# Kernel tuning notes

Hardware: AMD Instinct MI355X
Metric: run time of the kernel (lower is better)

The kernel has to match this reference:

```python
import jax, jax.numpy as jnp
import numpy as np

B = 131072   # batch
K = 3        # kernel size (= stride)
NP = 9       # num patches (9x9 image, 3x3 kernel, stride 3)
NU = 81      # num logic units/kernels
NOPS = 16    # real-valued binary logic ops


def setup_inputs() -> dict:
    key = jax.random.key(0)
    k1, k2, k3, k4 = jax.random.split(key, 4)
    x = jax.random.uniform(k1, (B, 1, 9, 9), dtype=jnp.float32)          # soft-binary image
    sel_a_logits = jax.random.normal(k2, (NU, K * K), dtype=jnp.float32)  # input-A selector per unit
    sel_b_logits = jax.random.normal(k3, (NU, K * K), dtype=jnp.float32)  # input-B selector per unit
    op_logits = jax.random.normal(k4, (NU, NOPS), dtype=jnp.float32)      # logic-op mixture per unit
    return {"x": x, "sel_a_logits": sel_a_logits, "sel_b_logits": sel_b_logits, "op_logits": op_logits}


def _soft_logic_mix(a, b, w):
    # a, b: [B, NU] soft-binary operands; w: [NU, 16] op mixture weights (broadcast over batch).
    # The 16 real-valued binary logic gates (Petersen et al. differentiable logic networks).
    ab = a * b
    return (w[:, 1] * ab
            + w[:, 2] * (a - ab)
            + w[:, 3] * a
            + w[:, 4] * (b - ab)
            + w[:, 5] * b
            + w[:, 6] * (a + b - 2.0 * ab)      # xor
            + w[:, 7] * (a + b - ab)            # or
            + w[:, 8] * (1.0 - (a + b - ab))    # nor
            + w[:, 9] * (1.0 - (a + b - 2.0 * ab))  # xnor
            + w[:, 10] * (1.0 - b)
            + w[:, 11] * (1.0 - b + ab)
            + w[:, 12] * (1.0 - a)
            + w[:, 13] * (1.0 - a + ab)
            + w[:, 14] * (1.0 - ab)             # nand
            + w[:, 15])                          # op 0 contributes 0


def reference(x, sel_a_logits, sel_b_logits, op_logits):
    b_sz = x.shape[0]
    img = x[:, 0]  # [B, 9, 9]
    # unfold(2,K,S).unfold(3,K,S) with S == K == 3 -> non-overlapping 3x3 patches, row-major patch order
    patches = img.reshape(b_sz, NP // K, K, NP // K, K)
    patches = patches.transpose(0, 1, 3, 2, 4).reshape(b_sz, NP, K * K)  # [B, 9, 9]
    # unit u uses patch u // kernels_per_pos (kernels_per_pos = 81 // 9 = 9)
    unit2patch = jnp.arange(NU) // (NU // NP)
    inp = patches[:, unit2patch]  # [B, 81, 9]
    a = jnp.einsum('bui,ui->bu', inp, jax.nn.softmax(sel_a_logits, axis=-1))  # [B, 81]
    b = jnp.einsum('bui,ui->bu', inp, jax.nn.softmax(sel_b_logits, axis=-1))  # [B, 81]
    w = jax.nn.softmax(op_logits, axis=-1)  # [81, 16]
    return _soft_logic_mix(a, b, w)  # [B, 81]
```

## Files before the change

### kernel.cpp

```cpp
#include <hip/hip_runtime.h>
#include <math.h>


#define NB      131072
#define NUNITS  81
#define BPB     64
#define THREADS 256
#define NBLK    (NB / BPB)
#define REC     24
#define CHUNKS  1296

__global__ __launch_bounds__(THREADS)
void logic_conv2d_kernel(const float* __restrict__ x,
                         const float* __restrict__ sa_logits,
                         const float* __restrict__ sb_logits,
                         const float* __restrict__ op_logits,
                         float* __restrict__ out)
{
    __shared__ float s_in [BPB * 81];
    __shared__ float s_out[BPB * 81];
    __shared__ float s_tab[NUNITS * REC];

    const int tid  = threadIdx.x;
    const int lane = tid & 63;
    const int wave = tid >> 6;
    const size_t b0 = (size_t)blockIdx.x * BPB;

    {
        const float4* gsrc = (const float4*)(x + b0 * 81);
        float4* s4 = (float4*)s_in;
        #pragma unroll
        for (int k = 0; k < 6; ++k) {
            int j = tid + k * THREADS;
            if (j < CHUNKS) s4[j] = gsrc[j];
        }
    }

    if (tid < 81) {
        const int u = tid;
        float v[9], m = -1e30f;
        #pragma unroll
        for (int i = 0; i < 9; ++i) { v[i] = sa_logits[u * 9 + i]; m = fmaxf(m, v[i]); }
        float s = 0.f;
        #pragma unroll
        for (int i = 0; i < 9; ++i) { v[i] = expf(v[i] - m); s += v[i]; }
        const float r = 1.f / s;
        #pragma unroll
        for (int i = 0; i < 9; ++i) s_tab[u * REC + i] = v[i] * r;
    } else if (tid < 162) {
        const int u = tid - 81;
        float v[9], m = -1e30f;
        #pragma unroll
        for (int i = 0; i < 9; ++i) { v[i] = sb_logits[u * 9 + i]; m = fmaxf(m, v[i]); }
        float s = 0.f;
        #pragma unroll
        for (int i = 0; i < 9; ++i) { v[i] = expf(v[i] - m); s += v[i]; }
        const float r = 1.f / s;
        #pragma unroll
        for (int i = 0; i < 9; ++i) s_tab[u * REC + 9 + i] = v[i] * r;
    } else if (tid < 243) {
        const int u = tid - 162;
        float v[16], m = -1e30f;
        #pragma unroll
        for (int i = 0; i < 16; ++i) { v[i] = op_logits[u * 16 + i]; m = fmaxf(m, v[i]); }
        float s = 0.f;
        #pragma unroll
        for (int i = 0; i < 16; ++i) { v[i] = expf(v[i] - m); s += v[i]; }
        const float r = 1.f / s;
        #pragma unroll
        for (int i = 0; i < 16; ++i) v[i] *= r;
        const float cab = v[1] - v[2] - v[4] - 2.f*v[6] - v[7] + v[8] + 2.f*v[9]
                        + v[11] + v[13] - v[14];
        const float ca  = v[2] + v[3] + v[6] + v[7] - v[8] - v[9] - v[12] - v[13];
        const float cb  = v[4] + v[5] + v[6] + v[7] - v[8] - v[9] - v[10] - v[11];
        const float c0  = v[8] + v[9] + v[10] + v[11] + v[12] + v[13] + v[14] + v[15];
        s_tab[u * REC + 18] = cab;
        s_tab[u * REC + 19] = ca;
        s_tab[u * REC + 20] = cb;
        s_tab[u * REC + 21] = c0;
    }

    __syncthreads();

    {
        const float* my_in = s_in + lane * 81;
        for (int u = wave; u < NUNITS; u += 4) {
            const int p    = u / 9;
            const int base = (p / 3) * 27 + (p % 3) * 3;
            const float i0 = my_in[base + 0],  i1 = my_in[base + 1],  i2 = my_in[base + 2];
            const float i3 = my_in[base + 9],  i4 = my_in[base + 10], i5 = my_in[base + 11];
            const float i6 = my_in[base + 18], i7 = my_in[base + 19], i8 = my_in[base + 20];
            const float* wr = s_tab + u * REC;
            const float a = i0*wr[0] + i1*wr[1] + i2*wr[2]
                          + i3*wr[3] + i4*wr[4] + i5*wr[5]
                          + i6*wr[6] + i7*wr[7] + i8*wr[8];
            const float b = i0*wr[9]  + i1*wr[10] + i2*wr[11]
                          + i3*wr[12] + i4*wr[13] + i5*wr[14]
                          + i6*wr[15] + i7*wr[16] + i8*wr[17];
            const float res = wr[21] + wr[19]*a + wr[20]*b + wr[18]*(a*b);
            s_out[lane * 81 + u] = res;
        }
    }

    __syncthreads();

    {
        const float4* s4 = (const float4*)s_out;
        float4* gdst = (float4*)(out + b0 * 81);
        #pragma unroll
        for (int k = 0; k < 6; ++k) {
            int j = tid + k * THREADS;
            if (j < CHUNKS) gdst[j] = s4[j];
        }
    }
}

extern "C" void kernel_launch(void* const* d_in, const int* in_sizes, int n_in,
                              void* d_out, int out_size, void* d_ws, size_t ws_size,
                              hipStream_t stream)
{
    const float* x  = (const float*)d_in[0];
    const float* sa = (const float*)d_in[1];
    const float* sb = (const float*)d_in[2];
    const float* op = (const float*)d_in[3];
    float* out = (float*)d_out;
    logic_conv2d_kernel<<<NBLK, THREADS, 0, stream>>>(x, sa, sb, op, out);
}
```

Measured before the change: 32.78 us.

## Split softmax prep into separate kernel and reuse one shared tile in main kernel

```diff
diff --git a/kernel.cpp b/kernel.cpp
--- a/kernel.cpp
+++ b/kernel.cpp
@@ -10,32 +10,13 @@
 #define REC     24
 #define CHUNKS  1296
 
-__global__ __launch_bounds__(THREADS)
-void logic_conv2d_kernel(const float* __restrict__ x,
-                         const float* __restrict__ sa_logits,
-                         const float* __restrict__ sb_logits,
-                         const float* __restrict__ op_logits,
-                         float* __restrict__ out)
+__global__ __launch_bounds__(256)
+void logic_prep_kernel(const float* __restrict__ sa_logits,
+                       const float* __restrict__ sb_logits,
+                       const float* __restrict__ op_logits,
+                       float* __restrict__ tab)
 {
-    __shared__ float s_in [BPB * 81];
-    __shared__ float s_out[BPB * 81];
-    __shared__ float s_tab[NUNITS * REC];
-
-    const int tid  = threadIdx.x;
-    const int lane = tid & 63;
-    const int wave = tid >> 6;
-    const size_t b0 = (size_t)blockIdx.x * BPB;
-
-    {
-        const float4* gsrc = (const float4*)(x + b0 * 81);
-        float4* s4 = (float4*)s_in;
-        #pragma unroll
-        for (int k = 0; k < 6; ++k) {
-            int j = tid + k * THREADS;
-            if (j < CHUNKS) s4[j] = gsrc[j];
-        }
-    }
-
+    const int tid = threadIdx.x;
     if (tid < 81) {
         const int u = tid;
         float v[9], m = -1e30f;
@@ -46,7 +27,7 @@
         for (int i = 0; i < 9; ++i) { v[i] = expf(v[i] - m); s += v[i]; }
         const float r = 1.f / s;
         #pragma unroll
-        for (int i = 0; i < 9; ++i) s_tab[u * REC + i] = v[i] * r;
+        for (int i = 0; i < 9; ++i) tab[u * REC + i] = v[i] * r;
     } else if (tid < 162) {
         const int u = tid - 81;
         float v[9], m = -1e30f;
@@ -57,7 +38,7 @@
         for (int i = 0; i < 9; ++i) { v[i] = expf(v[i] - m); s += v[i]; }
         const float r = 1.f / s;
         #pragma unroll
-        for (int i = 0; i < 9; ++i) s_tab[u * REC + 9 + i] = v[i] * r;
+        for (int i = 0; i < 9; ++i) tab[u * REC + 9 + i] = v[i] * r;
     } else if (tid < 243) {
         const int u = tid - 162;
         float v[16], m = -1e30f;
@@ -74,38 +55,78 @@
         const float ca  = v[2] + v[3] + v[6] + v[7] - v[8] - v[9] - v[12] - v[13];
         const float cb  = v[4] + v[5] + v[6] + v[7] - v[8] - v[9] - v[10] - v[11];
         const float c0  = v[8] + v[9] + v[10] + v[11] + v[12] + v[13] + v[14] + v[15];
-        s_tab[u * REC + 18] = cab;
-        s_tab[u * REC + 19] = ca;
-        s_tab[u * REC + 20] = cb;
-        s_tab[u * REC + 21] = c0;
+        tab[u * REC + 18] = cab;
+        tab[u * REC + 19] = ca;
+        tab[u * REC + 20] = cb;
+        tab[u * REC + 21] = c0;
+    }
+}
+
+__global__ __launch_bounds__(THREADS, 4)
+void logic_main_kernel(const float* __restrict__ x,
+                       const float* __restrict__ tab,
+                       float* __restrict__ out)
+{
+    __shared__ float s_tile[BPB * 81];
+
+    const int tid  = threadIdx.x;
+    const int lane = tid & 63;
+    const int wave = tid >> 6;
+    const size_t b0 = (size_t)blockIdx.x * BPB;
+
+    {
+        const float4* gsrc = (const float4*)(x + b0 * 81);
+        float4* s4 = (float4*)s_tile;
+        #pragma unroll
+        for (int k = 0; k < 6; ++k) {
+            int j = tid + k * THREADS;
+            if (j < CHUNKS) s4[j] = gsrc[j];
+        }
+    }
+    __syncthreads();
+
+    const int u0 = (wave * NUNITS) >> 2;
+    const int u1 = ((wave + 1) * NUNITS) >> 2;
+    const int p0 = u0 / 9;
+    const float* my_in = s_tile + lane * 81;
+
+    float in[3][9];
+    #pragma unroll
+    for (int pp = 0; pp < 3; ++pp) {
+        const int p    = p0 + pp;
+        const int base = (p / 3) * 27 + (p % 3) * 3;
+        #pragma unroll
+        for (int r = 0; r < 3; ++r) {
+            in[pp][r*3+0] = my_in[base + r*9 + 0];
+            in[pp][r*3+1] = my_in[base + r*9 + 1];
+            in[pp][r*3+2] = my_in[base + r*9 + 2];
+        }
     }
 
     __syncthreads();
 
-    {
-        const float* my_in = s_in + lane * 81;
-        for (int u = wave; u < NUNITS; u += 4) {
-            const int p    = u / 9;
-            const int base = (p / 3) * 27 + (p % 3) * 3;
-            const float i0 = my_in[base + 0],  i1 = my_in[base + 1],  i2 = my_in[base + 2];
-            const float i3 = my_in[base + 9],  i4 = my_in[base + 10], i5 = my_in[base + 11];
-            const float i6 = my_in[base + 18], i7 = my_in[base + 19], i8 = my_in[base + 20];
-            const float* wr = s_tab + u * REC;
-            const float a = i0*wr[0] + i1*wr[1] + i2*wr[2]
-                          + i3*wr[3] + i4*wr[4] + i5*wr[5]
-                          + i6*wr[6] + i7*wr[7] + i8*wr[8];
-            const float b = i0*wr[9]  + i1*wr[10] + i2*wr[11]
-                          + i3*wr[12] + i4*wr[13] + i5*wr[14]
-                          + i6*wr[15] + i7*wr[16] + i8*wr[17];
-            const float res = wr[21] + wr[19]*a + wr[20]*b + wr[18]*(a*b);
-            s_out[lane * 81 + u] = res;
+    #pragma unroll
+    for (int pp = 0; pp < 3; ++pp) {
+        const int p  = p0 + pp;
+        const int ua = (u0 > p * 9)     ? u0 : p * 9;
+        const int ub = (u1 < p * 9 + 9) ? u1 : p * 9 + 9;
+        for (int u = ua; u < ub; ++u) {
+            const int uu = __builtin_amdgcn_readfirstlane(u);
+            const float* __restrict__ wr = tab + (size_t)uu * REC;
+            const float a = in[pp][0]*wr[0] + in[pp][1]*wr[1] + in[pp][2]*wr[2]
+                          + in[pp][3]*wr[3] + in[pp][4]*wr[4] + in[pp][5]*wr[5]
+                          + in[pp][6]*wr[6] + in[pp][7]*wr[7] + in[pp][8]*wr[8];
+            const float b = in[pp][0]*wr[9]  + in[pp][1]*wr[10] + in[pp][2]*wr[11]
+                          + in[pp][3]*wr[12] + in[pp][4]*wr[13] + in[pp][5]*wr[14]
+                          + in[pp][6]*wr[15] + in[pp][7]*wr[16] + in[pp][8]*wr[17];
+            s_tile[lane * 81 + u] = wr[21] + wr[19]*a + wr[20]*b + wr[18]*(a*b);
         }
     }
 
     __syncthreads();
 
     {
-        const float4* s4 = (const float4*)s_out;
+        const float4* s4 = (const float4*)s_tile;
         float4* gdst = (float4*)(out + b0 * 81);
         #pragma unroll
         for (int k = 0; k < 6; ++k) {
@@ -123,6 +144,9 @@
     const float* sa = (const float*)d_in[1];
     const float* sb = (const float*)d_in[2];
     const float* op = (const float*)d_in[3];
-    float* out = (float*)d_out;
-    logic_conv2d_kernel<<<NBLK, THREADS, 0, stream>>>(x, sa, sb, op, out);
+    float* tab = (float*)d_ws;
+    float* outp = (float*)d_out;
+
+    logic_prep_kernel<<<1, 256, 0, stream>>>(sa, sb, op, tab);
+    logic_main_kernel<<<NBLK, THREADS, 0, stream>>>(x, tab, outp);
 }
```

Measured after the change: 33.84 us. 1.03x slower.
